# Performance work log

Measured on AMD Instinct MI355X. Metric: run time of the kernel, lower is better.

The kernel has to match this reference:

```python
import jax, jax.numpy as jnp
import numpy as np

DIM = 2048
N_HEADS = 32
N_KV_HEADS = 8
HEAD_DIM = DIM // N_HEADS
B, T = 2, 2048


def setup_inputs() -> dict:
    key = jax.random.key(0)
    ks = jax.random.split(key, 5)
    std = 0.02
    return {
        "x": jax.random.normal(ks[0], (B, T, DIM), dtype=jnp.float32),
        "wq": jax.random.normal(ks[1], (DIM, DIM), dtype=jnp.float32) * std,
        "wk": jax.random.normal(ks[2], (N_KV_HEADS * HEAD_DIM, DIM), dtype=jnp.float32) * std,
        "wv": jax.random.normal(ks[3], (N_KV_HEADS * HEAD_DIM, DIM), dtype=jnp.float32) * std,
        "wo": jax.random.normal(ks[4], (DIM, DIM), dtype=jnp.float32) * std,
    }


def _rope_tables(seq_len, head_dim, dtype):
    inv_freq = 1.0 / (10000.0 ** (jnp.arange(0, head_dim, 2, dtype=jnp.float32) / head_dim))
    t = jnp.arange(seq_len, dtype=jnp.float32)
    freqs = jnp.einsum("i,j->ij", t, inv_freq)          # [T, hd/2]
    emb = jnp.concatenate([freqs, freqs], axis=-1)       # [T, hd]
    return jnp.cos(emb).astype(dtype), jnp.sin(emb).astype(dtype)


def _rotate_half(x):
    h = x.shape[-1] // 2
    return jnp.concatenate([-x[..., h:], x[..., :h]], axis=-1)


def reference(x, wq, wk, wv, wo):
    Bc, Tc, C = x.shape
    q = (x @ wq.T).reshape(Bc, Tc, N_HEADS, HEAD_DIM).transpose(0, 2, 1, 3)      # [B,H,T,hd]
    k = (x @ wk.T).reshape(Bc, Tc, N_KV_HEADS, HEAD_DIM).transpose(0, 2, 1, 3)   # [B,Hk,T,hd]
    v = (x @ wv.T).reshape(Bc, Tc, N_KV_HEADS, HEAD_DIM).transpose(0, 2, 1, 3)

    cos, sin = _rope_tables(Tc, HEAD_DIM, x.dtype)  # [T,hd] broadcast over B,H
    q = q * cos + _rotate_half(q) * sin
    k = k * cos + _rotate_half(k) * sin

    rep = N_HEADS // N_KV_HEADS
    k = jnp.repeat(k, rep, axis=1)  # [B,H,T,hd]
    v = jnp.repeat(v, rep, axis=1)

    scale = 1.0 / np.sqrt(HEAD_DIM)
    scores = jnp.einsum("bhqd,bhkd->bhqk", q, k) * scale   # [B,H,T,T]
    causal = jnp.triu(jnp.ones((Tc, Tc), dtype=bool), k=1)
    scores = jnp.where(causal, jnp.asarray(-jnp.inf, scores.dtype), scores)
    attn = jax.nn.softmax(scores, axis=-1)
    out = jnp.einsum("bhqk,bhkd->bhqd", attn, v)           # [B,H,T,hd]
    out = out.transpose(0, 2, 1, 3).reshape(Bc, Tc, C)
    return out @ wo.T
```

## Files before the change

kernel.cpp:

```cpp
#include <hip/hip_runtime.h>


typedef unsigned short u16;
typedef __attribute__((ext_vector_type(8))) short bf16x8;
typedef __attribute__((ext_vector_type(4))) float f32x4;
typedef __attribute__((ext_vector_type(4))) unsigned short u16x4;

constexpr int T_SEQ = 2048;
constexpr int DIMC  = 2048;
constexpr int NHEAD = 32;
constexpr int HDIM  = 64;
constexpr int KVDIM = 512;
constexpr int BATCH = 2;

__device__ __forceinline__ u16 f2bf(float f) {
    union { float f; unsigned int i; } v; v.f = f;
    unsigned int r = v.i + 0x7FFFu + ((v.i >> 16) & 1u);
    return (u16)(r >> 16);
}

typedef __attribute__((address_space(1))) unsigned int as1_uint;
typedef __attribute__((address_space(3))) unsigned int as3_uint;
__device__ __forceinline__ void glds16(const u16* g, u16* l) {
    __builtin_amdgcn_global_load_lds((as1_uint*)(u16*)g, (as3_uint*)l, 16, 0, 0);
}

__global__ __launch_bounds__(256) void cvt5(const float* __restrict__ x,
                                            const float* __restrict__ wq,
                                            const float* __restrict__ wk,
                                            const float* __restrict__ wv,
                                            const float* __restrict__ wo,
                                            u16* __restrict__ xb,  u16* __restrict__ wqb,
                                            u16* __restrict__ wkb, u16* __restrict__ wvb,
                                            u16* __restrict__ wob) {
    constexpr int E0 = BATCH * T_SEQ * DIMC;
    constexpr int E1 = E0 + DIMC * DIMC;
    constexpr int E2 = E1 + KVDIM * DIMC;
    constexpr int E3 = E2 + KVDIM * DIMC;
    constexpr int E4 = E3 + DIMC * DIMC;
    for (int i = (blockIdx.x * 256 + threadIdx.x) * 4; i < E4; i += gridDim.x * 1024) {
        const float* s; u16* d; int off;
        if (i < E0)      { s = x;  d = xb;  off = 0;  }
        else if (i < E1) { s = wq; d = wqb; off = E0; }
        else if (i < E2) { s = wk; d = wkb; off = E1; }
        else if (i < E3) { s = wv; d = wvb; off = E2; }
        else             { s = wo; d = wob; off = E3; }
        f32x4 v = *(const f32x4*)(s + (i - off));
        u16x4 o;
        #pragma unroll
        for (int e = 0; e < 4; ++e) o[e] = f2bf(v[e]);
        *(u16x4*)(d + (i - off)) = o;
    }
}

template <bool OUTF32>
__device__ __forceinline__ void gemm_core(const u16* __restrict__ A,
                                          const u16* __restrict__ W,
                                          void* __restrict__ Cv,
                                          int rowBase, int colBase,
                                          int N, int K, bool rope) {
    __shared__ __align__(16) u16 As[128 * 32];
    __shared__ __align__(16) u16 Bs[128 * 32];

    const int tid  = threadIdx.x;
    const int lane = tid & 63;
    const int w    = tid >> 6;
    const int quad = lane >> 4;
    const int ln   = lane & 15;
    const int wm = (w >> 1) * 64;
    const int wn = (w & 1) * 64;

    f32x4 acc[4][4] = {};

    const int srow = lane >> 2;
    const int scol = (lane & 3) * 8;
    const u16* aC0 = A + (size_t)(rowBase + w * 16 + srow) * K + scol;
    const u16* aC1 = A + (size_t)(rowBase + (w + 4) * 16 + srow) * K + scol;
    const u16* bC0 = W + (size_t)(colBase + w * 16 + srow) * K + scol;
    const u16* bC1 = W + (size_t)(colBase + (w + 4) * 16 + srow) * K + scol;
    u16* asl0 = As + w * 512;
    u16* asl1 = As + (w + 4) * 512;
    u16* bsl0 = Bs + w * 512;
    u16* bsl1 = Bs + (w + 4) * 512;

    for (int kk = 0; kk < K; kk += 32) {
        __syncthreads();
        glds16(aC0 + kk, asl0);
        glds16(aC1 + kk, asl1);
        glds16(bC0 + kk, bsl0);
        glds16(bC1 + kk, bsl1);
        __syncthreads();

        bf16x8 bw[4];
        #pragma unroll
        for (int j = 0; j < 4; ++j) bw[j] = *(const bf16x8*)(Bs + (wn + j * 16 + ln) * 32 + quad * 8);
        #pragma unroll
        for (int i = 0; i < 4; ++i) {
            bf16x8 af = *(const bf16x8*)(As + (wm + i * 16 + ln) * 32 + quad * 8);
            #pragma unroll
            for (int j = 0; j < 4; ++j)
                acc[i][j] = __builtin_amdgcn_mfma_f32_16x16x32_bf16(af, bw[j], acc[i][j], 0, 0, 0);
        }
    }

    if (rope) {
        #pragma unroll
        for (int i = 0; i < 4; ++i) {
            #pragma unroll
            for (int j = 0; j < 2; ++j) {
                int d = j * 16 + ln;
                float invf = exp2f(-(float)d * (13.287712379549449f / 32.0f));
                #pragma unroll
                for (int r = 0; r < 4; ++r) {
                    int mrow = rowBase + wm + i * 16 + quad * 4 + r;
                    int t = mrow & (T_SEQ - 1);
                    float fr = (float)t * invf;
                    float sn, cs;
                    sincosf(fr, &sn, &cs);
                    float a0 = acc[i][j][r], a2 = acc[i][j + 2][r];
                    acc[i][j][r]     = a0 * cs - a2 * sn;
                    acc[i][j + 2][r] = a2 * cs + a0 * sn;
                }
            }
        }
    }

    #pragma unroll
    for (int i = 0; i < 4; ++i) {
        int mrow = rowBase + wm + i * 16 + quad * 4;
        #pragma unroll
        for (int j = 0; j < 4; ++j) {
            int n = colBase + wn + j * 16 + ln;
            #pragma unroll
            for (int r = 0; r < 4; ++r) {
                if constexpr (OUTF32)
                    ((float*)Cv)[(size_t)(mrow + r) * N + n] = acc[i][j][r];
                else
                    ((u16*)Cv)[(size_t)(mrow + r) * N + n] = f2bf(acc[i][j][r]);
            }
        }
    }
}

__global__ __launch_bounds__(256, 4) void qkv_gemm(const u16* __restrict__ xb,
                                                   const u16* __restrict__ wqb,
                                                   const u16* __restrict__ wkb,
                                                   const u16* __restrict__ wvb,
                                                   u16* __restrict__ Qb,
                                                   u16* __restrict__ Kb,
                                                   u16* __restrict__ Vb) {
    const int nb = blockIdx.x;
    const int rowBase = blockIdx.y * 128;
    const u16* W; u16* C; int colBase, N; bool rope;
    if (nb < 16)      { W = wqb; C = Qb; colBase = nb * 128;        N = DIMC;  rope = true; }
    else if (nb < 20) { W = wkb; C = Kb; colBase = (nb - 16) * 128; N = KVDIM; rope = true; }
    else              { W = wvb; C = Vb; colBase = (nb - 20) * 128; N = KVDIM; rope = false; }
    gemm_core<false>(xb, W, C, rowBase, colBase, N, DIMC, rope);
}

__global__ __launch_bounds__(256, 4) void gemm_f32out(const u16* __restrict__ A,
                                                      const u16* __restrict__ W,
                                                      float* __restrict__ C,
                                                      int N, int K) {
    gemm_core<true>(A, W, C, blockIdx.y * 128, blockIdx.x * 128, N, K, false);
}

__global__ __launch_bounds__(256) void transpose_v(const u16* __restrict__ V,
                                                   u16* __restrict__ Vt) {
    __shared__ __align__(16) u16 tile[32][33];
    const int x = threadIdx.x & 31;
    const int y = threadIdx.x >> 5;
    const int tok0 = blockIdx.y * 32;
    const int c0   = blockIdx.x * 32;
    #pragma unroll
    for (int yy = 0; yy < 32; yy += 8)
        tile[y + yy][x] = V[(size_t)(tok0 + y + yy) * KVDIM + c0 + x];
    __syncthreads();
    const int b  = tok0 >> 11;
    const int t0 = tok0 & (T_SEQ - 1);
    #pragma unroll
    for (int yy = 0; yy < 32; yy += 8)
        Vt[(size_t)(b * KVDIM + c0 + y + yy) * T_SEQ + t0 + x] = tile[x][y + yy];
}

__global__ __launch_bounds__(256) void attn(const u16* __restrict__ Q,
                                            const u16* __restrict__ Kx,
                                            const u16* __restrict__ Vt,
                                            u16* __restrict__ O) {
    __shared__ __align__(16) u16 Ks[64][72];
    __shared__ __align__(16) u16 Vs[64][72];
    __shared__ __align__(16) u16 Ps[2][4][16][72];

    const int tid  = threadIdx.x;
    const int lane = tid & 63;
    const int w    = tid >> 6;
    const int quad = lane >> 4;
    const int ln   = lane & 15;
    const int h    = blockIdx.y;
    const int b    = blockIdx.z;
    const int kvh  = h >> 2;

    const int srow = tid >> 2;
    const int scol = (tid & 3) * 16;
    const u16* kbase = Kx + (size_t)(b * T_SEQ + srow) * KVDIM + kvh * HDIM + scol;
    const u16* vbase = Vt + (size_t)(b * KVDIM + kvh * HDIM + srow) * T_SEQ;

    const float K1 = 0.125f * 1.4426950408889634f;
    const float K2 = 8.0f * 1.4426950408889634f;

    #pragma unroll
    for (int phase = 0; phase < 2; ++phase) {
        const int qt = phase ? (15 - (int)blockIdx.x) : (int)blockIdx.x;
        const int qbase = qt * 128;
        const int qr0[2] = { qbase + w * 16, qbase + 64 + w * 16 };

        bf16x8 aq[2][2];
        #pragma unroll
        for (int g = 0; g < 2; ++g) {
            const u16* qp = Q + (size_t)(b * T_SEQ + qr0[g] + ln) * DIMC + h * HDIM + quad * 8;
            aq[g][0] = *(const bf16x8*)qp;
            aq[g][1] = *(const bf16x8*)(qp + 32);
        }

        f32x4 o[2][4] = {};
        float lpart[2][4] = {};

        const int ktmax = 2 * qt + 1;
        for (int kt = 0; kt <= ktmax; ++kt) {
            const int k0 = kt * 64;
            __syncthreads();
            *(bf16x8*)&Ks[srow][scol]     = *(const bf16x8*)(kbase + (size_t)k0 * KVDIM);
            *(bf16x8*)&Ks[srow][scol + 8] = *(const bf16x8*)(kbase + (size_t)k0 * KVDIM + 8);
            *(bf16x8*)&Vs[srow][scol]     = *(const bf16x8*)(vbase + k0 + scol);
            *(bf16x8*)&Vs[srow][scol + 8] = *(const bf16x8*)(vbase + k0 + scol + 8);
            __syncthreads();

            #pragma unroll
            for (int g = 0; g < 2; ++g) {
                if (kt > 2 * qt + g) continue;
                const bool diag = (kt == 2 * qt + g);
                f32x4 s[4];
                #pragma unroll
                for (int st = 0; st < 4; ++st) {
                    f32x4 z = {};
                    s[st] = __builtin_amdgcn_mfma_f32_16x16x32_bf16(
                                aq[g][0], *(const bf16x8*)&Ks[st * 16 + ln][quad * 8], z, 0, 0, 0);
                    s[st] = __builtin_amdgcn_mfma_f32_16x16x32_bf16(
                                aq[g][1], *(const bf16x8*)&Ks[st * 16 + ln][32 + quad * 8], s[st], 0, 0, 0);
                }
                #pragma unroll
                for (int r = 0; r < 4; ++r) {
                    const int qg = qr0[g] + quad * 4 + r;
                    float e[4], rs = 0.0f;
                    #pragma unroll
                    for (int st = 0; st < 4; ++st) {
                        bool masked = diag && (k0 + st * 16 + ln > qg);
                        e[st] = masked ? 0.0f : exp2f(fmaf(s[st][r], K1, -K2));
                        rs += e[st];
                    }
                    lpart[g][r] += rs;
                    #pragma unroll
                    for (int st = 0; st < 4; ++st)
                        Ps[g][w][quad * 4 + r][st * 16 + ln] = f2bf(e[st]);
                }
            }
            __asm__ __volatile__("s_waitcnt lgkmcnt(0)" ::: "memory");

            #pragma unroll
            for (int g = 0; g < 2; ++g) {
                if (kt > 2 * qt + g) continue;
                bf16x8 pa0 = *(const bf16x8*)&Ps[g][w][ln][quad * 8];
                bf16x8 pa1 = *(const bf16x8*)&Ps[g][w][ln][32 + quad * 8];
                #pragma unroll
                for (int t = 0; t < 4; ++t) {
                    o[g][t] = __builtin_amdgcn_mfma_f32_16x16x32_bf16(
                                  pa0, *(const bf16x8*)&Vs[t * 16 + ln][quad * 8], o[g][t], 0, 0, 0);
                    o[g][t] = __builtin_amdgcn_mfma_f32_16x16x32_bf16(
                                  pa1, *(const bf16x8*)&Vs[t * 16 + ln][32 + quad * 8], o[g][t], 0, 0, 0);
                }
            }
        }

        #pragma unroll
        for (int g = 0; g < 2; ++g) {
            #pragma unroll
            for (int r = 0; r < 4; ++r) {
                float rs = lpart[g][r];
                rs += __shfl_xor(rs, 1);
                rs += __shfl_xor(rs, 2);
                rs += __shfl_xor(rs, 4);
                rs += __shfl_xor(rs, 8);
                float inv = 1.0f / rs;
                size_t obase = (size_t)(b * T_SEQ + qr0[g] + quad * 4 + r) * DIMC + h * HDIM;
                #pragma unroll
                for (int t = 0; t < 4; ++t)
                    O[obase + t * 16 + ln] = f2bf(o[g][t][r] * inv);
            }
        }
    }
}

extern "C" void kernel_launch(void* const* d_in, const int* in_sizes, int n_in,
                              void* d_out, int out_size, void* d_ws, size_t ws_size,
                              hipStream_t stream) {
    const float* x  = (const float*)d_in[0];
    const float* wq = (const float*)d_in[1];
    const float* wk = (const float*)d_in[2];
    const float* wv = (const float*)d_in[3];
    const float* wo = (const float*)d_in[4];
    float* out = (float*)d_out;

    char* ws = (char*)d_ws;
    constexpr size_t MB = 1024 * 1024;
    u16* Qb  = (u16*)(ws);
    u16* Kb  = (u16*)(ws + 16 * MB);
    u16* Vb  = (u16*)(ws + 20 * MB);
    u16* Vtb = (u16*)(ws + 24 * MB);
    u16* AOb = (u16*)(ws + 28 * MB);
    u16* xb  = AOb;
    u16* wqb = (u16*)(ws + 44 * MB);
    u16* wkb = (u16*)(ws + 52 * MB);
    u16* wvb = (u16*)(ws + 54 * MB);
    u16* wob = (u16*)(ws + 56 * MB);
    const int M = BATCH * T_SEQ;

    hipLaunchKernelGGL(cvt5, dim3(2048), dim3(256), 0, stream,
                       x, wq, wk, wv, wo, xb, wqb, wkb, wvb, wob);
    hipLaunchKernelGGL(qkv_gemm, dim3(24, M / 128), dim3(256), 0, stream,
                       xb, wqb, wkb, wvb, Qb, Kb, Vb);
    hipLaunchKernelGGL(transpose_v, dim3(KVDIM / 32, M / 32), dim3(256), 0, stream, Vb, Vtb);
    hipLaunchKernelGGL(attn, dim3(8, NHEAD, BATCH), dim3(256), 0, stream,
                       Qb, Kb, Vtb, AOb);
    hipLaunchKernelGGL(gemm_f32out, dim3(DIMC / 128, M / 128), dim3(256), 0, stream,
                       AOb, wob, out, DIMC, DIMC);
}
```

Before: 359.6 us.

## Shrink attention query tile to 64 rows and double grid blocks

The attention kernel now handles one 64-row query tile per phase instead of two 16-row groups per wave, so each block covers 64 query rows and the grid doubles to 16 blocks in x. The diagonal and off-diagonal key tiles get separate code paths, so the causal mask is only evaluated on the diagonal tile. P is converted to bf16 by truncation rather than round-to-nearest. This raises the number of blocks in flight and lowers register and LDS pressure. In exchange, each K/V tile load is reused by half as many query rows, which adds load and barrier overhead, and the truncation adds a slight bias to the probabilities.

```diff
diff --git a/kernel.cpp b/kernel.cpp
--- a/kernel.cpp
+++ b/kernel.cpp
@@ -17,6 +17,10 @@
     union { float f; unsigned int i; } v; v.f = f;
     unsigned int r = v.i + 0x7FFFu + ((v.i >> 16) & 1u);
     return (u16)(r >> 16);
+}
+__device__ __forceinline__ u16 f2bf_trunc(float f) {
+    union { float f; unsigned int i; } v; v.f = f;
+    return (u16)(v.i >> 16);
 }
 
 typedef __attribute__((address_space(1))) unsigned int as1_uint;
@@ -189,7 +193,7 @@
                                             u16* __restrict__ O) {
     __shared__ __align__(16) u16 Ks[64][72];
     __shared__ __align__(16) u16 Vs[64][72];
-    __shared__ __align__(16) u16 Ps[2][4][16][72];
+    __shared__ __align__(16) u16 Ps[4][16][72];
 
     const int tid  = threadIdx.x;
     const int lane = tid & 63;
@@ -210,23 +214,17 @@
 
     #pragma unroll
     for (int phase = 0; phase < 2; ++phase) {
-        const int qt = phase ? (15 - (int)blockIdx.x) : (int)blockIdx.x;
-        const int qbase = qt * 128;
-        const int qr0[2] = { qbase + w * 16, qbase + 64 + w * 16 };
-
-        bf16x8 aq[2][2];
-        #pragma unroll
-        for (int g = 0; g < 2; ++g) {
-            const u16* qp = Q + (size_t)(b * T_SEQ + qr0[g] + ln) * DIMC + h * HDIM + quad * 8;
-            aq[g][0] = *(const bf16x8*)qp;
-            aq[g][1] = *(const bf16x8*)(qp + 32);
-        }
-
-        f32x4 o[2][4] = {};
-        float lpart[2][4] = {};
-
-        const int ktmax = 2 * qt + 1;
-        for (int kt = 0; kt <= ktmax; ++kt) {
+        const int qt = phase ? (31 - (int)blockIdx.x) : (int)blockIdx.x;
+        const int qr0 = qt * 64 + w * 16;
+
+        const u16* qp = Q + (size_t)(b * T_SEQ + qr0 + ln) * DIMC + h * HDIM + quad * 8;
+        const bf16x8 aq0 = *(const bf16x8*)qp;
+        const bf16x8 aq1 = *(const bf16x8*)(qp + 32);
+
+        f32x4 o[4] = {};
+        float lpart[4] = {};
+
+        for (int kt = 0; kt <= qt; ++kt) {
             const int k0 = kt * 64;
             __syncthreads();
             *(bf16x8*)&Ks[srow][scol]     = *(const bf16x8*)(kbase + (size_t)k0 * KVDIM);
@@ -235,67 +233,72 @@
             *(bf16x8*)&Vs[srow][scol + 8] = *(const bf16x8*)(vbase + k0 + scol + 8);
             __syncthreads();
 
-            #pragma unroll
-            for (int g = 0; g < 2; ++g) {
-                if (kt > 2 * qt + g) continue;
-                const bool diag = (kt == 2 * qt + g);
-                f32x4 s[4];
-                #pragma unroll
-                for (int st = 0; st < 4; ++st) {
-                    f32x4 z = {};
-                    s[st] = __builtin_amdgcn_mfma_f32_16x16x32_bf16(
-                                aq[g][0], *(const bf16x8*)&Ks[st * 16 + ln][quad * 8], z, 0, 0, 0);
-                    s[st] = __builtin_amdgcn_mfma_f32_16x16x32_bf16(
-                                aq[g][1], *(const bf16x8*)&Ks[st * 16 + ln][32 + quad * 8], s[st], 0, 0, 0);
-                }
+            f32x4 s[4];
+            #pragma unroll
+            for (int st = 0; st < 4; ++st) {
+                f32x4 z = {};
+                s[st] = __builtin_amdgcn_mfma_f32_16x16x32_bf16(
+                            aq0, *(const bf16x8*)&Ks[st * 16 + ln][quad * 8], z, 0, 0, 0);
+                s[st] = __builtin_amdgcn_mfma_f32_16x16x32_bf16(
+                            aq1, *(const bf16x8*)&Ks[st * 16 + ln][32 + quad * 8], s[st], 0, 0, 0);
+            }
+
+            if (kt != qt) {
                 #pragma unroll
                 for (int r = 0; r < 4; ++r) {
-                    const int qg = qr0[g] + quad * 4 + r;
                     float e[4], rs = 0.0f;
                     #pragma unroll
                     for (int st = 0; st < 4; ++st) {
-                        bool masked = diag && (k0 + st * 16 + ln > qg);
+                        e[st] = exp2f(fmaf(s[st][r], K1, -K2));
+                        rs += e[st];
+                    }
+                    lpart[r] += rs;
+                    #pragma unroll
+                    for (int st = 0; st < 4; ++st)
+                        Ps[w][quad * 4 + r][st * 16 + ln] = f2bf_trunc(e[st]);
+                }
+            } else {
+                #pragma unroll
+                for (int r = 0; r < 4; ++r) {
+                    const int thr = w * 16 + quad * 4 + r;
+                    float e[4], rs = 0.0f;
+                    #pragma unroll
+                    for (int st = 0; st < 4; ++st) {
+                        bool masked = (st * 16 + ln > thr);
                         e[st] = masked ? 0.0f : exp2f(fmaf(s[st][r], K1, -K2));
                         rs += e[st];
                     }
-                    lpart[g][r] += rs;
+                    lpart[r] += rs;
                     #pragma unroll
                     for (int st = 0; st < 4; ++st)
-                        Ps[g][w][quad * 4 + r][st * 16 + ln] = f2bf(e[st]);
+                        Ps[w][quad * 4 + r][st * 16 + ln] = f2bf_trunc(e[st]);
                 }
             }
             __asm__ __volatile__("s_waitcnt lgkmcnt(0)" ::: "memory");
 
-            #pragma unroll
-            for (int g = 0; g < 2; ++g) {
-                if (kt > 2 * qt + g) continue;
-                bf16x8 pa0 = *(const bf16x8*)&Ps[g][w][ln][quad * 8];
-                bf16x8 pa1 = *(const bf16x8*)&Ps[g][w][ln][32 + quad * 8];
-                #pragma unroll
-                for (int t = 0; t < 4; ++t) {
-                    o[g][t] = __builtin_amdgcn_mfma_f32_16x16x32_bf16(
-                                  pa0, *(const bf16x8*)&Vs[t * 16 + ln][quad * 8], o[g][t], 0, 0, 0);
-                    o[g][t] = __builtin_amdgcn_mfma_f32_16x16x32_bf16(
-                                  pa1, *(const bf16x8*)&Vs[t * 16 + ln][32 + quad * 8], o[g][t], 0, 0, 0);
-                }
-            }
-        }
-
-        #pragma unroll
-        for (int g = 0; g < 2; ++g) {
-            #pragma unroll
-            for (int r = 0; r < 4; ++r) {
-                float rs = lpart[g][r];
-                rs += __shfl_xor(rs, 1);
-                rs += __shfl_xor(rs, 2);
-                rs += __shfl_xor(rs, 4);
-                rs += __shfl_xor(rs, 8);
-                float inv = 1.0f / rs;
-                size_t obase = (size_t)(b * T_SEQ + qr0[g] + quad * 4 + r) * DIMC + h * HDIM;
-                #pragma unroll
-                for (int t = 0; t < 4; ++t)
-                    O[obase + t * 16 + ln] = f2bf(o[g][t][r] * inv);
-            }
+            bf16x8 pa0 = *(const bf16x8*)&Ps[w][ln][quad * 8];
+            bf16x8 pa1 = *(const bf16x8*)&Ps[w][ln][32 + quad * 8];
+            #pragma unroll
+            for (int t = 0; t < 4; ++t) {
+                o[t] = __builtin_amdgcn_mfma_f32_16x16x32_bf16(
+                           pa0, *(const bf16x8*)&Vs[t * 16 + ln][quad * 8], o[t], 0, 0, 0);
+                o[t] = __builtin_amdgcn_mfma_f32_16x16x32_bf16(
+                           pa1, *(const bf16x8*)&Vs[t * 16 + ln][32 + quad * 8], o[t], 0, 0, 0);
+            }
+        }
+
+        #pragma unroll
+        for (int r = 0; r < 4; ++r) {
+            float rs = lpart[r];
+            rs += __shfl_xor(rs, 1);
+            rs += __shfl_xor(rs, 2);
+            rs += __shfl_xor(rs, 4);
+            rs += __shfl_xor(rs, 8);
+            float inv = 1.0f / rs;
+            size_t obase = (size_t)(b * T_SEQ + qr0 + quad * 4 + r) * DIMC + h * HDIM;
+            #pragma unroll
+            for (int t = 0; t < 4; ++t)
+                O[obase + t * 16 + ln] = f2bf(o[t][r] * inv);
         }
     }
 }
@@ -329,7 +332,7 @@
     hipLaunchKernelGGL(qkv_gemm, dim3(24, M / 128), dim3(256), 0, stream,
                        xb, wqb, wkb, wvb, Qb, Kb, Vb);
     hipLaunchKernelGGL(transpose_v, dim3(KVDIM / 32, M / 32), dim3(256), 0, stream, Vb, Vtb);
-    hipLaunchKernelGGL(attn, dim3(8, NHEAD, BATCH), dim3(256), 0, stream,
+    hipLaunchKernelGGL(attn, dim3(16, NHEAD, BATCH), dim3(256), 0, stream,
                        Qb, Kb, Vtb, AOb);
     hipLaunchKernelGGL(gemm_f32out, dim3(DIMC / 128, M / 128), dim3(256), 0, stream,
                        AOb, wob, out, DIMC, DIMC);
```

Measured after the change: 337.8 us. 1.06x faster.
